# Kernel tuning notes

Hardware: AMD Instinct MI355X
Metric: run time of the kernel (lower is better)

Reference implementation:

```python
import jax, jax.numpy as jnp
import numpy as np

N = 50000      # nodes
E = 800000     # edges (avg degree 16)
D = 64         # input/hidden dim
OUT = 1        # output head dim
ATT_SLOPE = 0.2   # PyG GATConv leaky_relu slope for attention logits
ACT_SLOPE = 0.01  # nn.LeakyReLU default slope


def _gat_layer(x, src, dst, W, a_src, a_dst, b, n):
    """PyG GATConv, heads=1, concat=True, with self-loops already in src/dst."""
    h = x @ W.T                                   # [n, D]
    logit = jax.nn.leaky_relu(h[src] @ a_src + h[dst] @ a_dst, ATT_SLOPE)  # [e]
    m = jax.ops.segment_max(logit, dst, num_segments=n)                    # per-dst max
    e = jnp.exp(logit - m[dst])
    denom = jax.ops.segment_sum(e, dst, num_segments=n)
    coef = e / denom[dst]                         # softmax over incoming edges
    out = jax.ops.segment_sum(coef[:, None] * h[src], dst, num_segments=n)
    return out + b


def setup_inputs() -> dict:
    key = jax.random.key(0)
    ks = jax.random.split(key, 16)
    s = 1.0 / np.sqrt(D)
    inp = {"x": jax.random.normal(ks[0], (N, D), dtype=jnp.float32)}
    for i in range(3):
        inp[f"W{i}"] = jax.random.normal(ks[1 + 4 * i], (D, D), dtype=jnp.float32) * s
        inp[f"a_src{i}"] = jax.random.normal(ks[2 + 4 * i], (D,), dtype=jnp.float32) * s
        inp[f"a_dst{i}"] = jax.random.normal(ks[3 + 4 * i], (D,), dtype=jnp.float32) * s
        inp[f"b{i}"] = jnp.zeros((D,), dtype=jnp.float32)
    inp["Wout"] = jax.random.normal(ks[13], (OUT, D), dtype=jnp.float32) * s
    inp["bout"] = jnp.zeros((OUT,), dtype=jnp.float32)
    inp["edge_index"] = jax.random.randint(ks[14], (2, E), 0, N, dtype=jnp.int64)
    return inp


def reference(x, W0, a_src0, a_dst0, b0, W1, a_src1, a_dst1, b1,
              W2, a_src2, a_dst2, b2, Wout, bout, edge_index):
    n = x.shape[0]
    loops = jnp.arange(n, dtype=edge_index.dtype)
    src = jnp.concatenate([edge_index[0], loops])  # GATConv add_self_loops=True
    dst = jnp.concatenate([edge_index[1], loops])
    act = lambda v: jax.nn.leaky_relu(v, ACT_SLOPE)
    h = act(_gat_layer(x, src, dst, W0, a_src0, a_dst0, b0, n))
    h = act(_gat_layer(h, src, dst, W1, a_src1, a_dst1, b1, n))
    h = act(_gat_layer(h, src, dst, W2, a_src2, a_dst2, b2, n))
    return h @ Wout.T + bout                       # [n, OUT]
```

## Files before the change

### kernel.cpp

```cpp
#include <hip/hip_runtime.h>
#include <hip/hip_fp16.h>

#define DD 64
#define ATT_SLOPE 0.2f
#define ACT_SLOPE 0.01f
#define GNPB 32
#define RCAP 64
#define PA_CHUNK 2048
#define BSH 9
#define BNODES 512
#define BCAP 10240

template <bool IN_HALF>
__device__ __forceinline__ void gemm_body(
        const void* __restrict__ in_, const float* __restrict__ W,
        const float* __restrict__ a_src, const float* __restrict__ a_dst,
        __half* __restrict__ h, float* __restrict__ as_out,
        float* __restrict__ ad_out, int n_nodes, int base, float* xin) {
    int t = threadIdx.x;
    int lane = t & 63;
    int w = t >> 6;
    if (IN_HALF) {
        const uint2* src = (const uint2*)in_;
        float4* xin4 = (float4*)xin;
        int lim = n_nodes * (DD / 4);
        #pragma unroll
        for (int i = 0; i < 2; ++i) {
            int idx = i * 256 + t;
            int gi = base * (DD / 4) + idx;
            uint2 v = {0, 0};
            if (gi < lim) v = src[gi];
            float2 f0 = __half22float2(*(const __half2*)&v.x);
            float2 f1 = __half22float2(*(const __half2*)&v.y);
            xin4[idx] = make_float4(f0.x, f0.y, f1.x, f1.y);
        }
    } else {
        float4* xin4 = (float4*)xin;
        const float4* src4 = (const float4*)in_;
        int lim = n_nodes * (DD / 4);
        #pragma unroll
        for (int i = 0; i < (GNPB * DD / 4) / 256; ++i) {
            int idx = i * 256 + t;
            int gi = base * (DD / 4) + idx;
            xin4[idx] = (gi < lim) ? src4[gi]
                                   : make_float4(0.f, 0.f, 0.f, 0.f);
        }
    }
    __syncthreads();

    int n0 = base + w * 8;
    if (n0 >= n_nodes) return;

    float asl = a_src[lane], adl = a_dst[lane];
    const float* wrow = W + (size_t)lane * 64;
    int rmax = n_nodes - n0; if (rmax > 8) rmax = 8;

    if (rmax == 8) {
        float a[8] = {0.f, 0.f, 0.f, 0.f, 0.f, 0.f, 0.f, 0.f};
        #pragma unroll
        for (int kq = 0; kq < 16; ++kq) {
            float4 wv = *(const float4*)(wrow + kq * 4);
            #pragma unroll
            for (int r = 0; r < 8; ++r) {
                float4 xv = *(const float4*)&xin[(w * 8 + r) * DD + kq * 4];
                a[r] = fmaf(xv.x, wv.x, a[r]); a[r] = fmaf(xv.y, wv.y, a[r]);
                a[r] = fmaf(xv.z, wv.z, a[r]); a[r] = fmaf(xv.w, wv.w, a[r]);
            }
        }
        #pragma unroll
        for (int r = 0; r < 8; ++r)
            h[(size_t)(n0 + r) * 64 + lane] = __float2half(a[r]);
        float s[16];
        #pragma unroll
        for (int r = 0; r < 8; ++r) { s[2 * r] = a[r] * asl; s[2 * r + 1] = a[r] * adl; }
        #pragma unroll
        for (int m = 32; m >= 1; m >>= 1) {
            #pragma unroll
            for (int i = 0; i < 16; ++i) s[i] += __shfl_xor(s[i], m, 64);
        }
        if (lane == 0) {
            #pragma unroll
            for (int r = 0; r < 8; ++r) {
                as_out[n0 + r] = s[2 * r];
                ad_out[n0 + r] = s[2 * r + 1];
            }
        }
    } else {
        for (int r = 0; r < rmax; ++r) {
            int node = n0 + r;
            float acc = 0.f;
            #pragma unroll
            for (int kq = 0; kq < 16; ++kq) {
                float4 wv = *(const float4*)(wrow + kq * 4);
                float4 xv = *(const float4*)&xin[(w * 8 + r) * DD + kq * 4];
                acc = fmaf(xv.x, wv.x, acc); acc = fmaf(xv.y, wv.y, acc);
                acc = fmaf(xv.z, wv.z, acc); acc = fmaf(xv.w, wv.w, acc);
            }
            h[(size_t)node * 64 + lane] = __float2half(acc);
            float s1 = acc * asl, s2 = acc * adl;
            #pragma unroll
            for (int m = 32; m >= 1; m >>= 1) {
                s1 += __shfl_xor(s1, m, 64);
                s2 += __shfl_xor(s2, m, 64);
            }
            if (lane == 0) { as_out[node] = s1; ad_out[node] = s2; }
        }
    }
}

__global__ __launch_bounds__(256) void gemm0_binA_kernel(
        const float* __restrict__ x, const float* __restrict__ W,
        const float* __restrict__ a_src, const float* __restrict__ a_dst,
        __half* __restrict__ h, float* __restrict__ as_out,
        float* __restrict__ ad_out, int n_nodes,
        const int* __restrict__ ei, int E,
        int* __restrict__ bcur, unsigned int* __restrict__ bucket_buf,
        int gemm_blocks) {
    __shared__ float xin[GNPB * DD];
    __shared__ int hist[128];
    __shared__ int gbase[128];
    int bid = blockIdx.x;
    if (bid < gemm_blocks) {
        gemm_body<false>(x, W, a_src, a_dst, h, as_out, ad_out, n_nodes,
                         bid * GNPB, xin);
        return;
    }
    int t = threadIdx.x;
    int base_e = (bid - gemm_blocks) * PA_CHUNK;
    int ET = E + n_nodes;
    if (t < 128) hist[t] = 0;
    __syncthreads();

    unsigned int ent[8];
    short eb[8];
    short ep[8];
    #pragma unroll
    for (int j = 0; j < 8; ++j) {
        int e = base_e + j * 256 + t;
        eb[j] = -1;
        if (e >= ET) continue;
        int s, d;
        if (e < E) { s = ei[e]; d = ei[E + e]; }
        else       { s = e - E; d = s; }
        int b = d >> BSH;
        ent[j] = (unsigned int)s | ((unsigned int)(d & (BNODES - 1)) << 16);
        eb[j] = (short)b;
        ep[j] = (short)atomicAdd(&hist[b], 1);
    }
    __syncthreads();
    if (t < 128) {
        int c = hist[t];
        gbase[t] = (c > 0) ? atomicAdd(&bcur[t], c) : 0;
    }
    __syncthreads();
    #pragma unroll
    for (int j = 0; j < 8; ++j) {
        if (eb[j] < 0) continue;
        int pos = gbase[eb[j]] + ep[j];
        if (pos < BCAP) bucket_buf[(size_t)eb[j] * BCAP + pos] = ent[j];
    }
}

__global__ __launch_bounds__(256) void binB_kernel(
        const unsigned int* __restrict__ bucket_buf, const int* __restrict__ bcur,
        int* __restrict__ counts, unsigned short* __restrict__ col_src,
        int n_nodes) {
    __shared__ int cur[BNODES];
    int b = blockIdx.x, t = threadIdx.x;
    for (int i = t; i < BNODES; i += 256) cur[i] = 0;
    __syncthreads();
    int cnt = bcur[b]; if (cnt > BCAP) cnt = BCAP;
    const unsigned int* buf = bucket_buf + (size_t)b * BCAP;
    for (int i = t; i < cnt; i += 256) {
        unsigned int en = buf[i];
        int s = en & 0xFFFF;
        int dl = en >> 16;
        int pos = atomicAdd(&cur[dl], 1);
        if (pos < RCAP)
            col_src[(((b << BSH) + dl) << 6) + pos] = (unsigned short)s;
    }
    __syncthreads();
    int n0 = b << BSH;
    for (int i = t; i < BNODES; i += 256) {
        int d = n0 + i;
        if (d < n_nodes) counts[d] = cur[i];
    }
}

__global__ __launch_bounds__(256) void gemm_alpha_kernel(
        const __half* __restrict__ in, const float* __restrict__ W,
        const float* __restrict__ a_src, const float* __restrict__ a_dst,
        __half* __restrict__ h, float* __restrict__ as_out,
        float* __restrict__ ad_out, int n_nodes) {
    __shared__ float xin[GNPB * DD];
    gemm_body<true>(in, W, a_src, a_dst, h, as_out, ad_out, n_nodes,
                    blockIdx.x * GNPB, xin);
}

template <bool FUSE_HEAD>
__global__ __launch_bounds__(256) void aggregate_kernel(
        const int* __restrict__ counts, const unsigned short* __restrict__ col_src,
        const __half* __restrict__ h, const float* __restrict__ as_arr,
        const float* __restrict__ ad_arr, const float* __restrict__ b,
        __half* __restrict__ out16, float* __restrict__ head_out,
        const float* __restrict__ Wout, const float* __restrict__ bout,
        int n_nodes) {
    int t = threadIdx.x;
    int w = t >> 6, lane = t & 63;
    int node = blockIdx.x * 4 + w;
    if (node >= n_nodes) return;
    int g = lane >> 3, u = lane & 7;

    int beg = node << 6;
    int cnt = __builtin_amdgcn_readfirstlane(counts[node]);
    if (cnt > RCAP) cnt = RCAP;
    int end = beg + cnt;
    float adn = ad_arr[node];

    float acc[8] = {0.f, 0.f, 0.f, 0.f, 0.f, 0.f, 0.f, 0.f};
    float lsum = 0.f;
    int e = beg + g;

    uint4 rA = {0, 0, 0, 0}, rB = {0, 0, 0, 0};
    float aA = 0.f, aB = 0.f;
    if (e < end) {
        int s = col_src[e];
        aA = as_arr[s];
        rA = *(const uint4*)(h + (size_t)s * 64 + u * 8);
    }
    if (e + 8 < end) {
        int s = col_src[e + 8];
        aB = as_arr[s];
        rB = *(const uint4*)(h + (size_t)s * 64 + u * 8);
    }
    while (e < end) {
        int e2 = e + 16;
        uint4 rC = {0, 0, 0, 0}; float aC = 0.f;
        if (e2 < end) {
            int s = col_src[e2];
            aC = as_arr[s];
            rC = *(const uint4*)(h + (size_t)s * 64 + u * 8);
        }
        float lg = aA + adn;
        lg = (lg >= 0.f) ? lg : ATT_SLOPE * lg;
        float p = __expf(lg);
        lsum += p;
        float2 f0 = __half22float2(*(const __half2*)&rA.x);
        float2 f1 = __half22float2(*(const __half2*)&rA.y);
        float2 f2 = __half22float2(*(const __half2*)&rA.z);
        float2 f3 = __half22float2(*(const __half2*)&rA.w);
        acc[0] = fmaf(p, f0.x, acc[0]); acc[1] = fmaf(p, f0.y, acc[1]);
        acc[2] = fmaf(p, f1.x, acc[2]); acc[3] = fmaf(p, f1.y, acc[3]);
        acc[4] = fmaf(p, f2.x, acc[4]); acc[5] = fmaf(p, f2.y, acc[5]);
        acc[6] = fmaf(p, f3.x, acc[6]); acc[7] = fmaf(p, f3.y, acc[7]);
        rA = rB; aA = aB;
        rB = rC; aB = aC;
        e += 8;
    }
    #pragma unroll
    for (int m = 8; m <= 32; m <<= 1) {
        #pragma unroll
        for (int i = 0; i < 8; ++i) acc[i] += __shfl_xor(acc[i], m, 64);
        lsum += __shfl_xor(lsum, m, 64);
    }
    float inv = 1.f / lsum;
    const float4 b0 = *(const float4*)(b + u * 8);
    const float4 b1 = *(const float4*)(b + u * 8 + 4);
    float o[8];
    o[0] = acc[0] * inv + b0.x; o[1] = acc[1] * inv + b0.y;
    o[2] = acc[2] * inv + b0.z; o[3] = acc[3] * inv + b0.w;
    o[4] = acc[4] * inv + b1.x; o[5] = acc[5] * inv + b1.y;
    o[6] = acc[6] * inv + b1.z; o[7] = acc[7] * inv + b1.w;
    #pragma unroll
    for (int i = 0; i < 8; ++i) o[i] = (o[i] >= 0.f) ? o[i] : ACT_SLOPE * o[i];

    if (FUSE_HEAD) {
        const float4 w0 = *(const float4*)(Wout + u * 8);
        const float4 w1 = *(const float4*)(Wout + u * 8 + 4);
        float pd = o[0] * w0.x + o[1] * w0.y + o[2] * w0.z + o[3] * w0.w
                 + o[4] * w1.x + o[5] * w1.y + o[6] * w1.z + o[7] * w1.w;
        #pragma unroll
        for (int m = 1; m <= 4; m <<= 1) pd += __shfl_xor(pd, m, 64);
        if (lane == 0) head_out[node] = pd + bout[0];
    } else if (g == 0) {
        __half2 p0 = __floats2half2_rn(o[0], o[1]);
        __half2 p1 = __floats2half2_rn(o[2], o[3]);
        __half2 p2 = __floats2half2_rn(o[4], o[5]);
        __half2 p3 = __floats2half2_rn(o[6], o[7]);
        uint4 pv;
        pv.x = *(unsigned int*)&p0; pv.y = *(unsigned int*)&p1;
        pv.z = *(unsigned int*)&p2; pv.w = *(unsigned int*)&p3;
        *(uint4*)(out16 + ((size_t)node << 6) + u * 8) = pv;
    }
}


extern "C" void kernel_launch(void* const* d_in, const int* in_sizes, int n_in,
                              void* d_out, int out_size, void* d_ws, size_t ws_size,
                              hipStream_t stream) {
    const float* x     = (const float*)d_in[0];
    const float* W[3]  = {(const float*)d_in[1], (const float*)d_in[5], (const float*)d_in[9]};
    const float* as[3] = {(const float*)d_in[2], (const float*)d_in[6], (const float*)d_in[10]};
    const float* ad[3] = {(const float*)d_in[3], (const float*)d_in[7], (const float*)d_in[11]};
    const float* bv[3] = {(const float*)d_in[4], (const float*)d_in[8], (const float*)d_in[12]};
    const float* Wout  = (const float*)d_in[13];
    const float* bout  = (const float*)d_in[14];
    const int*   ei    = (const int*)d_in[15];

    const int N  = in_sizes[0] / DD;
    const int E  = in_sizes[15] / 2;
    const int ET = E + N;
    const int NBUCK = (N + BNODES - 1) >> BSH;

    char* ws = (char*)d_ws;
    size_t off = 0;
    auto alloc = [&](size_t bytes) {
        void* p = ws + off;
        off = (off + bytes + 255) & ~(size_t)255;
        return p;
    };
    unsigned short* col_src = (unsigned short*)alloc((size_t)N * RCAP * 2);
    int*    counts  = (int*)alloc((size_t)N * 4);
    int*    bcur    = (int*)alloc(512 * 4);
    float*  asA     = (float*)alloc((size_t)N * 4);
    float*  adA     = (float*)alloc((size_t)N * 4);
    float*  asB     = (float*)alloc((size_t)N * 4);
    float*  adB     = (float*)alloc((size_t)N * 4);
    __half* hA      = (__half*)alloc((size_t)N * DD * 2);
    __half* hB      = (__half*)alloc((size_t)N * DD * 2);
    __half* obuf16  = (__half*)alloc((size_t)N * DD * 2);
    unsigned int* bucket_buf = (unsigned int*)alloc((size_t)NBUCK * BCAP * 4);
    (void)ws_size;

    int gridG = (N + GNPB - 1) / GNPB;
    int nA    = (ET + PA_CHUNK - 1) / PA_CHUNK;
    int grid4 = (N + 3) / 4;

    hipMemsetAsync(bcur, 0, 512 * 4, stream);
    gemm0_binA_kernel<<<gridG + nA, 256, 0, stream>>>(
        x, W[0], as[0], ad[0], hA, asA, adA, N,
        ei, E, bcur, bucket_buf, gridG);
    binB_kernel<<<NBUCK, 256, 0, stream>>>(bucket_buf, bcur, counts, col_src, N);

    aggregate_kernel<false><<<grid4, 256, 0, stream>>>(
        counts, col_src, hA, asA, adA, bv[0], obuf16,
        nullptr, nullptr, nullptr, N);
    gemm_alpha_kernel<<<gridG, 256, 0, stream>>>(obuf16, W[1], as[1], ad[1],
                                                 hB, asB, adB, N);
    aggregate_kernel<false><<<grid4, 256, 0, stream>>>(
        counts, col_src, hB, asB, adB, bv[1], obuf16,
        nullptr, nullptr, nullptr, N);
    gemm_alpha_kernel<<<gridG, 256, 0, stream>>>(obuf16, W[2], as[2], ad[2],
                                                 hA, asA, adA, N);
    aggregate_kernel<true><<<grid4, 256, 0, stream>>>(
        counts, col_src, hA, asA, adA, bv[2], nullptr,
        (float*)d_out, Wout, bout, N);
}
```

Measured before the change: 256.2 us.

## Fuse next-layer GEMM into aggregation and replace two-pass binning with global atomics

The separate gemm_alpha kernels are removed. Each aggregate wave now multiplies its activated output row by the next layer's W using lane shuffles, and writes h, a_src and a_dst for the next layer directly. This drops the fp16 intermediate buffer round trip and two launches. The two-pass bucketed CSR build (binA plus binB) is also replaced by one pass doing a global atomicAdd on per-node counts, which removes a kernel and the bucket buffer but adds heavy global atomic contention. Edge order within each row becomes nondeterministic, and the per-node GEMM reads W rows from global memory in every wave.

```diff
diff --git a/kernel.cpp b/kernel.cpp
--- a/kernel.cpp
+++ b/kernel.cpp
@@ -7,44 +7,24 @@
 #define GNPB 32
 #define RCAP 64
 #define PA_CHUNK 2048
-#define BSH 9
-#define BNODES 512
-#define BCAP 10240
-
-template <bool IN_HALF>
+
 __device__ __forceinline__ void gemm_body(
-        const void* __restrict__ in_, const float* __restrict__ W,
+        const float* __restrict__ in, const float* __restrict__ W,
         const float* __restrict__ a_src, const float* __restrict__ a_dst,
         __half* __restrict__ h, float* __restrict__ as_out,
         float* __restrict__ ad_out, int n_nodes, int base, float* xin) {
     int t = threadIdx.x;
     int lane = t & 63;
     int w = t >> 6;
-    if (IN_HALF) {
-        const uint2* src = (const uint2*)in_;
-        float4* xin4 = (float4*)xin;
-        int lim = n_nodes * (DD / 4);
-        #pragma unroll
-        for (int i = 0; i < 2; ++i) {
-            int idx = i * 256 + t;
-            int gi = base * (DD / 4) + idx;
-            uint2 v = {0, 0};
-            if (gi < lim) v = src[gi];
-            float2 f0 = __half22float2(*(const __half2*)&v.x);
-            float2 f1 = __half22float2(*(const __half2*)&v.y);
-            xin4[idx] = make_float4(f0.x, f0.y, f1.x, f1.y);
-        }
-    } else {
-        float4* xin4 = (float4*)xin;
-        const float4* src4 = (const float4*)in_;
-        int lim = n_nodes * (DD / 4);
-        #pragma unroll
-        for (int i = 0; i < (GNPB * DD / 4) / 256; ++i) {
-            int idx = i * 256 + t;
-            int gi = base * (DD / 4) + idx;
-            xin4[idx] = (gi < lim) ? src4[gi]
-                                   : make_float4(0.f, 0.f, 0.f, 0.f);
-        }
+    float4* xin4 = (float4*)xin;
+    const float4* src4 = (const float4*)in;
+    int lim = n_nodes * (DD / 4);
+    #pragma unroll
+    for (int i = 0; i < (GNPB * DD / 4) / 256; ++i) {
+        int idx = i * 256 + t;
+        int gi = base * (DD / 4) + idx;
+        xin4[idx] = (gi < lim) ? src4[gi]
+                               : make_float4(0.f, 0.f, 0.f, 0.f);
     }
     __syncthreads();
 
@@ -114,87 +94,29 @@
         __half* __restrict__ h, float* __restrict__ as_out,
         float* __restrict__ ad_out, int n_nodes,
         const int* __restrict__ ei, int E,
-        int* __restrict__ bcur, unsigned int* __restrict__ bucket_buf,
+        int* __restrict__ counts, unsigned short* __restrict__ col_src,
         int gemm_blocks) {
     __shared__ float xin[GNPB * DD];
-    __shared__ int hist[128];
-    __shared__ int gbase[128];
     int bid = blockIdx.x;
     if (bid < gemm_blocks) {
-        gemm_body<false>(x, W, a_src, a_dst, h, as_out, ad_out, n_nodes,
-                         bid * GNPB, xin);
+        gemm_body(x, W, a_src, a_dst, h, as_out, ad_out, n_nodes,
+                  bid * GNPB, xin);
         return;
     }
     int t = threadIdx.x;
     int base_e = (bid - gemm_blocks) * PA_CHUNK;
     int ET = E + n_nodes;
-    if (t < 128) hist[t] = 0;
-    __syncthreads();
-
-    unsigned int ent[8];
-    short eb[8];
-    short ep[8];
-    #pragma unroll
-    for (int j = 0; j < 8; ++j) {
+    #pragma unroll
+    for (int j = 0; j < PA_CHUNK / 256; ++j) {
         int e = base_e + j * 256 + t;
-        eb[j] = -1;
-        if (e >= ET) continue;
+        if (e >= ET) break;
         int s, d;
         if (e < E) { s = ei[e]; d = ei[E + e]; }
         else       { s = e - E; d = s; }
-        int b = d >> BSH;
-        ent[j] = (unsigned int)s | ((unsigned int)(d & (BNODES - 1)) << 16);
-        eb[j] = (short)b;
-        ep[j] = (short)atomicAdd(&hist[b], 1);
-    }
-    __syncthreads();
-    if (t < 128) {
-        int c = hist[t];
-        gbase[t] = (c > 0) ? atomicAdd(&bcur[t], c) : 0;
-    }
-    __syncthreads();
-    #pragma unroll
-    for (int j = 0; j < 8; ++j) {
-        if (eb[j] < 0) continue;
-        int pos = gbase[eb[j]] + ep[j];
-        if (pos < BCAP) bucket_buf[(size_t)eb[j] * BCAP + pos] = ent[j];
-    }
-}
-
-__global__ __launch_bounds__(256) void binB_kernel(
-        const unsigned int* __restrict__ bucket_buf, const int* __restrict__ bcur,
-        int* __restrict__ counts, unsigned short* __restrict__ col_src,
-        int n_nodes) {
-    __shared__ int cur[BNODES];
-    int b = blockIdx.x, t = threadIdx.x;
-    for (int i = t; i < BNODES; i += 256) cur[i] = 0;
-    __syncthreads();
-    int cnt = bcur[b]; if (cnt > BCAP) cnt = BCAP;
-    const unsigned int* buf = bucket_buf + (size_t)b * BCAP;
-    for (int i = t; i < cnt; i += 256) {
-        unsigned int en = buf[i];
-        int s = en & 0xFFFF;
-        int dl = en >> 16;
-        int pos = atomicAdd(&cur[dl], 1);
+        int pos = atomicAdd(&counts[d], 1);
         if (pos < RCAP)
-            col_src[(((b << BSH) + dl) << 6) + pos] = (unsigned short)s;
-    }
-    __syncthreads();
-    int n0 = b << BSH;
-    for (int i = t; i < BNODES; i += 256) {
-        int d = n0 + i;
-        if (d < n_nodes) counts[d] = cur[i];
-    }
-}
-
-__global__ __launch_bounds__(256) void gemm_alpha_kernel(
-        const __half* __restrict__ in, const float* __restrict__ W,
-        const float* __restrict__ a_src, const float* __restrict__ a_dst,
-        __half* __restrict__ h, float* __restrict__ as_out,
-        float* __restrict__ ad_out, int n_nodes) {
-    __shared__ float xin[GNPB * DD];
-    gemm_body<true>(in, W, a_src, a_dst, h, as_out, ad_out, n_nodes,
-                    blockIdx.x * GNPB, xin);
+            col_src[((size_t)d << 6) + pos] = (unsigned short)s;
+    }
 }
 
 template <bool FUSE_HEAD>
@@ -202,9 +124,11 @@
         const int* __restrict__ counts, const unsigned short* __restrict__ col_src,
         const __half* __restrict__ h, const float* __restrict__ as_arr,
         const float* __restrict__ ad_arr, const float* __restrict__ b,
-        __half* __restrict__ out16, float* __restrict__ head_out,
-        const float* __restrict__ Wout, const float* __restrict__ bout,
-        int n_nodes) {
+        const float* __restrict__ Wn, const float* __restrict__ an_src,
+        const float* __restrict__ an_dst, __half* __restrict__ h_next,
+        float* __restrict__ as_next, float* __restrict__ ad_next,
+        float* __restrict__ head_out, const float* __restrict__ Wout,
+        const float* __restrict__ bout, int n_nodes) {
     int t = threadIdx.x;
     int w = t >> 6, lane = t & 63;
     int node = blockIdx.x * 4 + w;
@@ -282,15 +206,36 @@
         #pragma unroll
         for (int m = 1; m <= 4; m <<= 1) pd += __shfl_xor(pd, m, 64);
         if (lane == 0) head_out[node] = pd + bout[0];
-    } else if (g == 0) {
-        __half2 p0 = __floats2half2_rn(o[0], o[1]);
-        __half2 p1 = __floats2half2_rn(o[2], o[3]);
-        __half2 p2 = __floats2half2_rn(o[4], o[5]);
-        __half2 p3 = __floats2half2_rn(o[6], o[7]);
-        uint4 pv;
-        pv.x = *(unsigned int*)&p0; pv.y = *(unsigned int*)&p1;
-        pv.z = *(unsigned int*)&p2; pv.w = *(unsigned int*)&p3;
-        *(uint4*)(out16 + ((size_t)node << 6) + u * 8) = pv;
+    } else {
+        int j = lane;
+        const float* wrow = Wn + (size_t)j * 64;
+        float hacc = 0.f;
+        #pragma unroll
+        for (int ub = 0; ub < 8; ++ub) {
+            float4 w0 = *(const float4*)(wrow + ub * 8);
+            float4 w1 = *(const float4*)(wrow + ub * 8 + 4);
+            float x0 = __shfl(o[0], ub, 64);
+            float x1 = __shfl(o[1], ub, 64);
+            float x2 = __shfl(o[2], ub, 64);
+            float x3 = __shfl(o[3], ub, 64);
+            float x4 = __shfl(o[4], ub, 64);
+            float x5 = __shfl(o[5], ub, 64);
+            float x6 = __shfl(o[6], ub, 64);
+            float x7 = __shfl(o[7], ub, 64);
+            hacc = fmaf(x0, w0.x, hacc); hacc = fmaf(x1, w0.y, hacc);
+            hacc = fmaf(x2, w0.z, hacc); hacc = fmaf(x3, w0.w, hacc);
+            hacc = fmaf(x4, w1.x, hacc); hacc = fmaf(x5, w1.y, hacc);
+            hacc = fmaf(x6, w1.z, hacc); hacc = fmaf(x7, w1.w, hacc);
+        }
+        h_next[((size_t)node << 6) + j] = __float2half(hacc);
+        float s1 = hacc * an_src[j];
+        float s2 = hacc * an_dst[j];
+        #pragma unroll
+        for (int m = 32; m >= 1; m >>= 1) {
+            s1 += __shfl_xor(s1, m, 64);
+            s2 += __shfl_xor(s2, m, 64);
+        }
+        if (lane == 0) { as_next[node] = s1; ad_next[node] = s2; }
     }
 }
 
@@ -310,7 +255,6 @@
     const int N  = in_sizes[0] / DD;
     const int E  = in_sizes[15] / 2;
     const int ET = E + N;
-    const int NBUCK = (N + BNODES - 1) >> BSH;
 
     char* ws = (char*)d_ws;
     size_t off = 0;
@@ -321,38 +265,33 @@
     };
     unsigned short* col_src = (unsigned short*)alloc((size_t)N * RCAP * 2);
     int*    counts  = (int*)alloc((size_t)N * 4);
-    int*    bcur    = (int*)alloc(512 * 4);
     float*  asA     = (float*)alloc((size_t)N * 4);
     float*  adA     = (float*)alloc((size_t)N * 4);
     float*  asB     = (float*)alloc((size_t)N * 4);
     float*  adB     = (float*)alloc((size_t)N * 4);
     __half* hA      = (__half*)alloc((size_t)N * DD * 2);
     __half* hB      = (__half*)alloc((size_t)N * DD * 2);
-    __half* obuf16  = (__half*)alloc((size_t)N * DD * 2);
-    unsigned int* bucket_buf = (unsigned int*)alloc((size_t)NBUCK * BCAP * 4);
     (void)ws_size;
 
     int gridG = (N + GNPB - 1) / GNPB;
     int nA    = (ET + PA_CHUNK - 1) / PA_CHUNK;
     int grid4 = (N + 3) / 4;
 
-    hipMemsetAsync(bcur, 0, 512 * 4, stream);
+    hipMemsetAsync(counts, 0, (size_t)N * 4, stream);
     gemm0_binA_kernel<<<gridG + nA, 256, 0, stream>>>(
         x, W[0], as[0], ad[0], hA, asA, adA, N,
-        ei, E, bcur, bucket_buf, gridG);
-    binB_kernel<<<NBUCK, 256, 0, stream>>>(bucket_buf, bcur, counts, col_src, N);
+        ei, E, counts, col_src, gridG);
 
     aggregate_kernel<false><<<grid4, 256, 0, stream>>>(
-        counts, col_src, hA, asA, adA, bv[0], obuf16,
+        counts, col_src, hA, asA, adA, bv[0],
+        W[1], as[1], ad[1], hB, asB, adB,
         nullptr, nullptr, nullptr, N);
-    gemm_alpha_kernel<<<gridG, 256, 0, stream>>>(obuf16, W[1], as[1], ad[1],
-                                                 hB, asB, adB, N);
     aggregate_kernel<false><<<grid4, 256, 0, stream>>>(
-        counts, col_src, hB, asB, adB, bv[1], obuf16,
+        counts, col_src, hB, asB, adB, bv[1],
+        W[2], as[2], ad[2], hA, asA, adA,
         nullptr, nullptr, nullptr, N);
-    gemm_alpha_kernel<<<gridG, 256, 0, stream>>>(obuf16, W[2], as[2], ad[2],
-                                                 hA, asA, adA, N);
     aggregate_kernel<true><<<grid4, 256, 0, stream>>>(
-        counts, col_src, hA, asA, adA, bv[2], nullptr,
+        counts, col_src, hA, asA, adA, bv[2],
+        nullptr, nullptr, nullptr, nullptr, nullptr, nullptr,
         (float*)d_out, Wout, bout, N);
 }
```

Measured after the change: 382.9 us. 49.5% more time.

## Replace two-pass bucketed CSR build with direct global-atomic scatter

Applied to the files above, without the earlier changes.

Removes the two-stage binning (block-local histogram into per-bucket buffers, then a second kernel scattering into per-node slots) and instead has each edge do a global atomicAdd on its destination counter and write its source directly into the padded per-node slot array. This drops one kernel launch and the intermediate bucket buffer round trip. In exchange it issues one random global atomic per edge and scattered 2-byte writes, which may contend more than the LDS-atomic approach. Edge slot order within a node becomes nondeterministic, as before.

```diff
diff --git a/kernel.cpp b/kernel.cpp
--- a/kernel.cpp
+++ b/kernel.cpp
@@ -7,9 +7,6 @@
 #define GNPB 32
 #define RCAP 64
 #define PA_CHUNK 2048
-#define BSH 9
-#define BNODES 512
-#define BCAP 10240
 
 template <bool IN_HALF>
 __device__ __forceinline__ void gemm_body(
@@ -114,11 +111,9 @@
         __half* __restrict__ h, float* __restrict__ as_out,
         float* __restrict__ ad_out, int n_nodes,
         const int* __restrict__ ei, int E,
-        int* __restrict__ bcur, unsigned int* __restrict__ bucket_buf,
+        int* __restrict__ counts, unsigned short* __restrict__ col_src,
         int gemm_blocks) {
     __shared__ float xin[GNPB * DD];
-    __shared__ int hist[128];
-    __shared__ int gbase[128];
     int bid = blockIdx.x;
     if (bid < gemm_blocks) {
         gemm_body<false>(x, W, a_src, a_dst, h, as_out, ad_out, n_nodes,
@@ -128,62 +123,16 @@
     int t = threadIdx.x;
     int base_e = (bid - gemm_blocks) * PA_CHUNK;
     int ET = E + n_nodes;
-    if (t < 128) hist[t] = 0;
-    __syncthreads();
-
-    unsigned int ent[8];
-    short eb[8];
-    short ep[8];
     #pragma unroll
-    for (int j = 0; j < 8; ++j) {
+    for (int j = 0; j < PA_CHUNK / 256; ++j) {
         int e = base_e + j * 256 + t;
-        eb[j] = -1;
-        if (e >= ET) continue;
+        if (e >= ET) break;
         int s, d;
         if (e < E) { s = ei[e]; d = ei[E + e]; }
         else       { s = e - E; d = s; }
-        int b = d >> BSH;
-        ent[j] = (unsigned int)s | ((unsigned int)(d & (BNODES - 1)) << 16);
-        eb[j] = (short)b;
-        ep[j] = (short)atomicAdd(&hist[b], 1);
-    }
-    __syncthreads();
-    if (t < 128) {
-        int c = hist[t];
-        gbase[t] = (c > 0) ? atomicAdd(&bcur[t], c) : 0;
-    }
-    __syncthreads();
-    #pragma unroll
-    for (int j = 0; j < 8; ++j) {
-        if (eb[j] < 0) continue;
-        int pos = gbase[eb[j]] + ep[j];
-        if (pos < BCAP) bucket_buf[(size_t)eb[j] * BCAP + pos] = ent[j];
-    }
-}
-
-__global__ __launch_bounds__(256) void binB_kernel(
-        const unsigned int* __restrict__ bucket_buf, const int* __restrict__ bcur,
-        int* __restrict__ counts, unsigned short* __restrict__ col_src,
-        int n_nodes) {
-    __shared__ int cur[BNODES];
-    int b = blockIdx.x, t = threadIdx.x;
-    for (int i = t; i < BNODES; i += 256) cur[i] = 0;
-    __syncthreads();
-    int cnt = bcur[b]; if (cnt > BCAP) cnt = BCAP;
-    const unsigned int* buf = bucket_buf + (size_t)b * BCAP;
-    for (int i = t; i < cnt; i += 256) {
-        unsigned int en = buf[i];
-        int s = en & 0xFFFF;
-        int dl = en >> 16;
-        int pos = atomicAdd(&cur[dl], 1);
+        int pos = atomicAdd(&counts[d], 1);
         if (pos < RCAP)
-            col_src[(((b << BSH) + dl) << 6) + pos] = (unsigned short)s;
-    }
-    __syncthreads();
-    int n0 = b << BSH;
-    for (int i = t; i < BNODES; i += 256) {
-        int d = n0 + i;
-        if (d < n_nodes) counts[d] = cur[i];
+            col_src[((size_t)d << 6) + pos] = (unsigned short)s;
     }
 }
 
@@ -310,7 +259,6 @@
     const int N  = in_sizes[0] / DD;
     const int E  = in_sizes[15] / 2;
     const int ET = E + N;
-    const int NBUCK = (N + BNODES - 1) >> BSH;
 
     char* ws = (char*)d_ws;
     size_t off = 0;
@@ -321,7 +269,6 @@
     };
     unsigned short* col_src = (unsigned short*)alloc((size_t)N * RCAP * 2);
     int*    counts  = (int*)alloc((size_t)N * 4);
-    int*    bcur    = (int*)alloc(512 * 4);
     float*  asA     = (float*)alloc((size_t)N * 4);
     float*  adA     = (float*)alloc((size_t)N * 4);
     float*  asB     = (float*)alloc((size_t)N * 4);
@@ -329,18 +276,16 @@
     __half* hA      = (__half*)alloc((size_t)N * DD * 2);
     __half* hB      = (__half*)alloc((size_t)N * DD * 2);
     __half* obuf16  = (__half*)alloc((size_t)N * DD * 2);
-    unsigned int* bucket_buf = (unsigned int*)alloc((size_t)NBUCK * BCAP * 4);
     (void)ws_size;
 
     int gridG = (N + GNPB - 1) / GNPB;
     int nA    = (ET + PA_CHUNK - 1) / PA_CHUNK;
     int grid4 = (N + 3) / 4;
 
-    hipMemsetAsync(bcur, 0, 512 * 4, stream);
+    hipMemsetAsync(counts, 0, (size_t)N * 4, stream);
     gemm0_binA_kernel<<<gridG + nA, 256, 0, stream>>>(
         x, W[0], as[0], ad[0], hA, asA, adA, N,
-        ei, E, bcur, bucket_buf, gridG);
-    binB_kernel<<<NBUCK, 256, 0, stream>>>(bucket_buf, bcur, counts, col_src, N);
+        ei, E, counts, col_src, gridG);
 
     aggregate_kernel<false><<<grid4, 256, 0, stream>>>(
         counts, col_src, hA, asA, adA, bv[0], obuf16,
```

Measured after the change: 270.0 us. 1.05x slower.

## Recompute source attention scores in aggregation and use finer dst buckets

Applied to the files above, without the earlier changes.

The per-node source attention score is no longer precomputed in the GEMM and stored. The aggregation kernel now computes it on the fly as a dot product of the already-gathered fp16 feature slice with a_src, reduced with three lane shuffles. This removes a dependent random gather of as_arr per edge and a global write per node, at the cost of extra FMAs and shuffles in the inner loop; it also uses fp16-rounded h for the score. Separately, the binning bucket size drops from 512 to 256 nodes, with 256 buckets and the histogram aliased onto the xin shared buffer.

```diff
diff --git a/kernel.cpp b/kernel.cpp
--- a/kernel.cpp
+++ b/kernel.cpp
@@ -7,16 +7,16 @@
 #define GNPB 32
 #define RCAP 64
 #define PA_CHUNK 2048
-#define BSH 9
-#define BNODES 512
-#define BCAP 10240
+#define BSH 8
+#define BNODES 256
+#define BCAP 5888
 
 template <bool IN_HALF>
 __device__ __forceinline__ void gemm_body(
         const void* __restrict__ in_, const float* __restrict__ W,
-        const float* __restrict__ a_src, const float* __restrict__ a_dst,
-        __half* __restrict__ h, float* __restrict__ as_out,
-        float* __restrict__ ad_out, int n_nodes, int base, float* xin) {
+        const float* __restrict__ a_dst,
+        __half* __restrict__ h, float* __restrict__ ad_out,
+        int n_nodes, int base, float* xin) {
     int t = threadIdx.x;
     int lane = t & 63;
     int w = t >> 6;
@@ -51,7 +51,7 @@
     int n0 = base + w * 8;
     if (n0 >= n_nodes) return;
 
-    float asl = a_src[lane], adl = a_dst[lane];
+    float adl = a_dst[lane];
     const float* wrow = W + (size_t)lane * 64;
     int rmax = n_nodes - n0; if (rmax > 8) rmax = 8;
 
@@ -70,20 +70,17 @@
         #pragma unroll
         for (int r = 0; r < 8; ++r)
             h[(size_t)(n0 + r) * 64 + lane] = __float2half(a[r]);
-        float s[16];
-        #pragma unroll
-        for (int r = 0; r < 8; ++r) { s[2 * r] = a[r] * asl; s[2 * r + 1] = a[r] * adl; }
+        float s[8];
+        #pragma unroll
+        for (int r = 0; r < 8; ++r) s[r] = a[r] * adl;
         #pragma unroll
         for (int m = 32; m >= 1; m >>= 1) {
             #pragma unroll
-            for (int i = 0; i < 16; ++i) s[i] += __shfl_xor(s[i], m, 64);
+            for (int i = 0; i < 8; ++i) s[i] += __shfl_xor(s[i], m, 64);
         }
         if (lane == 0) {
             #pragma unroll
-            for (int r = 0; r < 8; ++r) {
-                as_out[n0 + r] = s[2 * r];
-                ad_out[n0 + r] = s[2 * r + 1];
-            }
+            for (int r = 0; r < 8; ++r) ad_out[n0 + r] = s[r];
         }
     } else {
         for (int r = 0; r < rmax; ++r) {
@@ -97,38 +94,33 @@
                 acc = fmaf(xv.z, wv.z, acc); acc = fmaf(xv.w, wv.w, acc);
             }
             h[(size_t)node * 64 + lane] = __float2half(acc);
-            float s1 = acc * asl, s2 = acc * adl;
-            #pragma unroll
-            for (int m = 32; m >= 1; m >>= 1) {
-                s1 += __shfl_xor(s1, m, 64);
-                s2 += __shfl_xor(s2, m, 64);
-            }
-            if (lane == 0) { as_out[node] = s1; ad_out[node] = s2; }
+            float s2 = acc * adl;
+            #pragma unroll
+            for (int m = 32; m >= 1; m >>= 1) s2 += __shfl_xor(s2, m, 64);
+            if (lane == 0) ad_out[node] = s2;
         }
     }
 }
 
 __global__ __launch_bounds__(256) void gemm0_binA_kernel(
         const float* __restrict__ x, const float* __restrict__ W,
-        const float* __restrict__ a_src, const float* __restrict__ a_dst,
-        __half* __restrict__ h, float* __restrict__ as_out,
-        float* __restrict__ ad_out, int n_nodes,
+        const float* __restrict__ a_dst,
+        __half* __restrict__ h, float* __restrict__ ad_out, int n_nodes,
         const int* __restrict__ ei, int E,
         int* __restrict__ bcur, unsigned int* __restrict__ bucket_buf,
         int gemm_blocks) {
     __shared__ float xin[GNPB * DD];
-    __shared__ int hist[128];
-    __shared__ int gbase[128];
+    int* hist  = (int*)xin;
+    int* gbase = hist + 256;
     int bid = blockIdx.x;
     if (bid < gemm_blocks) {
-        gemm_body<false>(x, W, a_src, a_dst, h, as_out, ad_out, n_nodes,
-                         bid * GNPB, xin);
+        gemm_body<false>(x, W, a_dst, h, ad_out, n_nodes, bid * GNPB, xin);
         return;
     }
     int t = threadIdx.x;
     int base_e = (bid - gemm_blocks) * PA_CHUNK;
     int ET = E + n_nodes;
-    if (t < 128) hist[t] = 0;
+    hist[t] = 0;
     __syncthreads();
 
     unsigned int ent[8];
@@ -148,7 +140,7 @@
         ep[j] = (short)atomicAdd(&hist[b], 1);
     }
     __syncthreads();
-    if (t < 128) {
+    {
         int c = hist[t];
         gbase[t] = (c > 0) ? atomicAdd(&bcur[t], c) : 0;
     }
@@ -167,7 +159,7 @@
         int n_nodes) {
     __shared__ int cur[BNODES];
     int b = blockIdx.x, t = threadIdx.x;
-    for (int i = t; i < BNODES; i += 256) cur[i] = 0;
+    if (t < BNODES) cur[t] = 0;
     __syncthreads();
     int cnt = bcur[b]; if (cnt > BCAP) cnt = BCAP;
     const unsigned int* buf = bucket_buf + (size_t)b * BCAP;
@@ -181,26 +173,24 @@
     }
     __syncthreads();
     int n0 = b << BSH;
-    for (int i = t; i < BNODES; i += 256) {
-        int d = n0 + i;
-        if (d < n_nodes) counts[d] = cur[i];
+    if (t < BNODES) {
+        int d = n0 + t;
+        if (d < n_nodes) counts[d] = cur[t];
     }
 }
 
 __global__ __launch_bounds__(256) void gemm_alpha_kernel(
         const __half* __restrict__ in, const float* __restrict__ W,
-        const float* __restrict__ a_src, const float* __restrict__ a_dst,
-        __half* __restrict__ h, float* __restrict__ as_out,
-        float* __restrict__ ad_out, int n_nodes) {
+        const float* __restrict__ a_dst,
+        __half* __restrict__ h, float* __restrict__ ad_out, int n_nodes) {
     __shared__ float xin[GNPB * DD];
-    gemm_body<true>(in, W, a_src, a_dst, h, as_out, ad_out, n_nodes,
-                    blockIdx.x * GNPB, xin);
+    gemm_body<true>(in, W, a_dst, h, ad_out, n_nodes, blockIdx.x * GNPB, xin);
 }
 
 template <bool FUSE_HEAD>
 __global__ __launch_bounds__(256) void aggregate_kernel(
         const int* __restrict__ counts, const unsigned short* __restrict__ col_src,
-        const __half* __restrict__ h, const float* __restrict__ as_arr,
+        const __half* __restrict__ h, const float* __restrict__ a_src,
         const float* __restrict__ ad_arr, const float* __restrict__ b,
         __half* __restrict__ out16, float* __restrict__ head_out,
         const float* __restrict__ Wout, const float* __restrict__ bout,
@@ -216,45 +206,48 @@
     if (cnt > RCAP) cnt = RCAP;
     int end = beg + cnt;
     float adn = ad_arr[node];
+    const float4 as0 = *(const float4*)(a_src + u * 8);
+    const float4 as1 = *(const float4*)(a_src + u * 8 + 4);
 
     float acc[8] = {0.f, 0.f, 0.f, 0.f, 0.f, 0.f, 0.f, 0.f};
     float lsum = 0.f;
     int e = beg + g;
 
     uint4 rA = {0, 0, 0, 0}, rB = {0, 0, 0, 0};
-    float aA = 0.f, aB = 0.f;
     if (e < end) {
         int s = col_src[e];
-        aA = as_arr[s];
         rA = *(const uint4*)(h + (size_t)s * 64 + u * 8);
     }
     if (e + 8 < end) {
         int s = col_src[e + 8];
-        aB = as_arr[s];
         rB = *(const uint4*)(h + (size_t)s * 64 + u * 8);
     }
     while (e < end) {
         int e2 = e + 16;
-        uint4 rC = {0, 0, 0, 0}; float aC = 0.f;
+        uint4 rC = {0, 0, 0, 0};
         if (e2 < end) {
             int s = col_src[e2];
-            aC = as_arr[s];
             rC = *(const uint4*)(h + (size_t)s * 64 + u * 8);
         }
-        float lg = aA + adn;
-        lg = (lg >= 0.f) ? lg : ATT_SLOPE * lg;
-        float p = __expf(lg);
-        lsum += p;
         float2 f0 = __half22float2(*(const __half2*)&rA.x);
         float2 f1 = __half22float2(*(const __half2*)&rA.y);
         float2 f2 = __half22float2(*(const __half2*)&rA.z);
         float2 f3 = __half22float2(*(const __half2*)&rA.w);
+        float das = f0.x * as0.x + f0.y * as0.y + f1.x * as0.z + f1.y * as0.w
+                  + f2.x * as1.x + f2.y * as1.y + f3.x * as1.z + f3.y * as1.w;
+        das += __shfl_xor(das, 1, 64);
+        das += __shfl_xor(das, 2, 64);
+        das += __shfl_xor(das, 4, 64);
+        float lg = das + adn;
+        lg = (lg >= 0.f) ? lg : ATT_SLOPE * lg;
+        float p = __expf(lg);
+        lsum += p;
         acc[0] = fmaf(p, f0.x, acc[0]); acc[1] = fmaf(p, f0.y, acc[1]);
         acc[2] = fmaf(p, f1.x, acc[2]); acc[3] = fmaf(p, f1.y, acc[3]);
         acc[4] = fmaf(p, f2.x, acc[4]); acc[5] = fmaf(p, f2.y, acc[5]);
         acc[6] = fmaf(p, f3.x, acc[6]); acc[7] = fmaf(p, f3.y, acc[7]);
-        rA = rB; aA = aB;
-        rB = rC; aB = aC;
+        rA = rB;
+        rB = rC;
         e += 8;
     }
     #pragma unroll
@@ -321,10 +314,8 @@
     };
     unsigned short* col_src = (unsigned short*)alloc((size_t)N * RCAP * 2);
     int*    counts  = (int*)alloc((size_t)N * 4);
-    int*    bcur    = (int*)alloc(512 * 4);
-    float*  asA     = (float*)alloc((size_t)N * 4);
+    int*    bcur    = (int*)alloc(256 * 4);
     float*  adA     = (float*)alloc((size_t)N * 4);
-    float*  asB     = (float*)alloc((size_t)N * 4);
     float*  adB     = (float*)alloc((size_t)N * 4);
     __half* hA      = (__half*)alloc((size_t)N * DD * 2);
     __half* hB      = (__half*)alloc((size_t)N * DD * 2);
@@ -336,23 +327,20 @@
     int nA    = (ET + PA_CHUNK - 1) / PA_CHUNK;
     int grid4 = (N + 3) / 4;
 
-    hipMemsetAsync(bcur, 0, 512 * 4, stream);
+    hipMemsetAsync(bcur, 0, 256 * 4, stream);
     gemm0_binA_kernel<<<gridG + nA, 256, 0, stream>>>(
-        x, W[0], as[0], ad[0], hA, asA, adA, N,
-        ei, E, bcur, bucket_buf, gridG);
+        x, W[0], ad[0], hA, adA, N, ei, E, bcur, bucket_buf, gridG);
     binB_kernel<<<NBUCK, 256, 0, stream>>>(bucket_buf, bcur, counts, col_src, N);
 
     aggregate_kernel<false><<<grid4, 256, 0, stream>>>(
-        counts, col_src, hA, asA, adA, bv[0], obuf16,
+        counts, col_src, hA, as[0], adA, bv[0], obuf16,
         nullptr, nullptr, nullptr, N);
-    gemm_alpha_kernel<<<gridG, 256, 0, stream>>>(obuf16, W[1], as[1], ad[1],
-                                                 hB, asB, adB, N);
+    gemm_alpha_kernel<<<gridG, 256, 0, stream>>>(obuf16, W[1], ad[1], hB, adB, N);
     aggregate_kernel<false><<<grid4, 256, 0, stream>>>(
-        counts, col_src, hB, asB, adB, bv[1], obuf16,
+        counts, col_src, hB, as[1], adB, bv[1], obuf16,
         nullptr, nullptr, nullptr, N);
-    gemm_alpha_kernel<<<gridG, 256, 0, stream>>>(obuf16, W[2], as[2], ad[2],
-                                                 hA, asA, adA, N);
+    gemm_alpha_kernel<<<gridG, 256, 0, stream>>>(obuf16, W[2], ad[2], hA, adA, N);
     aggregate_kernel<true><<<grid4, 256, 0, stream>>>(
-        counts, col_src, hA, asA, adA, bv[2], nullptr,
+        counts, col_src, hA, as[2], adA, bv[2], nullptr,
         (float*)d_out, Wout, bout, N);
 }
```

Result: faster. 247.3 us (-3.5%).
